# Performance work log

Measured on AMD Instinct MI355X. Metric: run time of the kernel, lower is better.

## Reference

```python
import jax, jax.numpy as jnp
import numpy as np

SPACE_TOKEN = 63
STRIDE = 2
B, F, T, W = 16, 512, 8192, 4096


def setup_inputs() -> dict:
    key = jax.random.key(0)
    k1, k2, k3 = jax.random.split(key, 3)
    word_preds = jax.random.normal(k1, (B, F, W), dtype=jnp.float32)
    char_features = jax.random.normal(k2, (B, F, T), dtype=jnp.float32)
    target_chars = jax.random.randint(k3, (B, T), 0, 64, dtype=jnp.int32)
    return {"word_preds": word_preds, "char_features": char_features, "target_chars": target_chars}


def _per_batch(wp, cf, ch):
    # wp: (F, W) predicted word vectors; cf: (F, T) char features; ch: (T,) char ids
    Tn = ch.shape[0]
    Wn = wp.shape[1]
    space = ch == SPACE_TOKEN
    cum = jnp.cumsum(space.astype(jnp.int32))  # spaces seen up to and including t
    n_spaces = cum[-1]
    # span k lives strictly between space #k and space #(k+1) (0-indexed spaces).
    # a non-space char at t (with cum[t] spaces before it) belongs to span cum[t]-1.
    seg = jnp.where(space | (cum == 0), Tn, cum - 1)  # invalid chars -> dump segment Tn
    counts = jax.ops.segment_sum(jnp.ones((Tn,), jnp.int32), seg, num_segments=Tn + 1)[:Tn]
    sums = jax.ops.segment_sum(cf.T, seg, num_segments=Tn + 1)[:Tn]  # (Tn, F)
    # position of space #k via one-hot scatter of positions
    sid = jnp.where(space, cum - 1, Tn)
    pos_k = jax.ops.segment_sum(jnp.arange(Tn, dtype=jnp.int32), sid, num_segments=Tn + 1)[:Tn]
    word_pos = pos_k // STRIDE
    k = jnp.arange(Tn, dtype=jnp.int32)
    # valid span: a following space exists, span non-empty, word_pos in range
    valid = (k < n_spaces - 1) & (counts > 0) & (word_pos < Wn)
    target = sums / jnp.maximum(counts, 1).astype(sums.dtype)[:, None]  # span mean (detached in torch)
    target = jax.lax.stop_gradient(target)
    pred = wp[:, jnp.clip(word_pos, 0, Wn - 1)].T  # (Tn, F) gather of predictions
    mse = jnp.mean((pred - target) ** 2, axis=1)  # per-span mean over feat dim (F.mse_loss)
    return jnp.sum(jnp.where(valid, mse, 0.0)), jnp.sum(valid.astype(jnp.int32))


def reference(word_preds, char_features, target_chars):
    losses, cnts = jax.vmap(_per_batch)(word_preds, char_features, target_chars)
    total = jnp.sum(losses)
    count = jnp.sum(cnts)
    return jnp.where(count > 0, total / jnp.maximum(count, 1).astype(total.dtype), jnp.float32(0.0))
```

## Files before the change

### kernel.cpp

```cpp
#include <hip/hip_runtime.h>


constexpr int SPACE_TOKEN = 63;
constexpr int B = 16;
constexpr int FDIM = 512;
constexpr int T = 8192;
constexpr int W = 4096;
constexpr int ROWS = 8;
constexpr int NPART = B * FDIM / ROWS;

__global__ __launch_bounds__(1024) void k_find_spaces(
    const int* __restrict__ chars, int* __restrict__ spacePos,
    int* __restrict__ nspaces, int* __restrict__ validCount) {
  const int b = blockIdx.x;
  const int* c = chars + (size_t)b * T;
  int* pos = spacePos + (size_t)b * T;
  __shared__ int s_wtot[16];
  __shared__ int s_wpair[16];
  const int tid = threadIdx.x;
  const int lane = tid & 63;
  const int wid = tid >> 6;

  const int4* c4 = (const int4*)c;
  const int4 a0 = c4[tid * 2];
  const int4 a1 = c4[tid * 2 + 1];
  int v[8] = {a0.x, a0.y, a0.z, a0.w, a1.x, a1.y, a1.z, a1.w};
  int nxt = SPACE_TOKEN + 1;
  if (tid < 1023) nxt = c[tid * 8 + 8];

  int cnt = 0, pairs = 0;
  #pragma unroll
  for (int i = 0; i < 8; ++i) cnt += (v[i] == SPACE_TOKEN);
  #pragma unroll
  for (int i = 0; i < 7; ++i)
    pairs += (v[i] == SPACE_TOKEN) && (v[i + 1] == SPACE_TOKEN);
  pairs += (v[7] == SPACE_TOKEN) && (nxt == SPACE_TOKEN);

  int inc = cnt, pr = pairs;
  #pragma unroll
  for (int o = 1; o < 64; o <<= 1) {
    const int n = __shfl_up(inc, o);
    if (lane >= o) inc += n;
  }
  #pragma unroll
  for (int o = 32; o > 0; o >>= 1) pr += __shfl_down(pr, o);
  if (lane == 63) s_wtot[wid] = inc;
  if (lane == 0) s_wpair[wid] = pr;
  __syncthreads();
  int wexc = 0;
  for (int w = 0; w < wid; ++w) wexc += s_wtot[w];
  int base = wexc + inc - cnt;
  #pragma unroll
  for (int i = 0; i < 8; ++i)
    if (v[i] == SPACE_TOKEN) pos[base++] = tid * 8 + i;
  if (tid == 0) {
    int S = 0, P = 0;
    for (int w = 0; w < 16; ++w) { S += s_wtot[w]; P += s_wpair[w]; }
    nspaces[b] = S;
    validCount[b] = (S > 1 ? S - 1 : 0) - P;
  }
}

__device__ __forceinline__ int swz(int u) { return u ^ ((u >> 3) & 7); }

#define BAR_VM8() do { asm volatile("s_waitcnt vmcnt(8)" ::: "memory"); \
  __builtin_amdgcn_s_barrier(); asm volatile("" ::: "memory"); } while (0)
#define BAR_VM0() do { asm volatile("s_waitcnt vmcnt(0)" ::: "memory"); \
  __builtin_amdgcn_s_barrier(); asm volatile("" ::: "memory"); } while (0)
#define BAR_LGKM() do { asm volatile("s_waitcnt lgkmcnt(0)" ::: "memory"); \
  __builtin_amdgcn_s_barrier(); asm volatile("" ::: "memory"); } while (0)

__device__ __forceinline__ void stage_row(const float4* __restrict__ src,
                                          float* dst, int tid, int wid) {
  float4* d4 = (float4*)dst;
  #pragma unroll
  for (int i = 0; i < 8; ++i) {
    const int u = i * 256 + tid;
    const float4* gsrc = src + swz(u);
    float4* ldst = d4 + (i * 256 + wid * 64);
    __builtin_amdgcn_global_load_lds(
        (const __attribute__((address_space(1))) void*)(const void*)gsrc,
        (__attribute__((address_space(3))) void*)(void*)ldst, 16, 0, 0);
  }
}

__global__ __launch_bounds__(256) void k_span_loss(
    const float* __restrict__ wp, const float* __restrict__ cf,
    const int* __restrict__ spacePos, const int* __restrict__ nspaces,
    float* __restrict__ partials) {
  const int blk = blockIdx.x;
  const int row0 = blk * ROWS;
  const int b = row0 >> 9;
  __shared__ alignas(16) float buf[2][T];
  __shared__ alignas(16) float csum[256];
  __shared__ alignas(16) float cexc[256];
  __shared__ float s_red[4];
  const int tid = threadIdx.x;
  const int lane = tid & 63;
  const int wid = tid >> 6;

  stage_row((const float4*)(cf + (size_t)row0 * T), buf[0], tid, wid);

  const int* pos = spacePos + (size_t)b * T;
  const int S = nspaces[b];
  const int p0r = pos[tid];
  const int p1r = pos[tid + 1];
  const int gidx = (p0r >> 1) & (W - 1);
  float wv[ROWS];
  #pragma unroll
  for (int r = 0; r < ROWS; ++r)
    wv[r] = wp[(size_t)(row0 + r) * W + gidx];

  float acc = 0.f;
  #pragma unroll 1
  for (int r = 0; r < ROWS; ++r) {
    if (r + 1 < ROWS)
      stage_row((const float4*)(cf + (size_t)(row0 + r + 1) * T),
                buf[(r + 1) & 1], tid, wid);
    if (r + 1 < ROWS) { BAR_VM8(); } else { BAR_VM0(); }

    float* rowf = buf[r & 1];
    float4* r4 = (float4*)rowf;

    float4 v[8];
    #pragma unroll
    for (int i = 0; i < 8; ++i) v[i] = r4[swz(tid * 8 + i)];
    float run = 0.f;
    #pragma unroll
    for (int i = 0; i < 8; ++i) {
      v[i].x = (run += v[i].x);
      v[i].y = (run += v[i].y);
      v[i].z = (run += v[i].z);
      v[i].w = (run += v[i].w);
    }
    #pragma unroll
    for (int i = 0; i < 8; ++i) r4[swz(tid * 8 + i)] = v[i];
    csum[tid] = run;
    BAR_LGKM();

    if (tid < 64) {
      const float4 sv = ((const float4*)csum)[tid];
      const float l1 = sv.x + sv.y;
      const float l2 = l1 + sv.z;
      const float tot = l2 + sv.w;
      float inc = tot;
      #pragma unroll
      for (int o = 1; o < 64; o <<= 1) {
        const float n = __shfl_up(inc, o);
        if (tid >= o) inc += n;
      }
      const float exc = inc - tot;
      ((float4*)cexc)[tid] = make_float4(exc, exc + sv.x, exc + l1, exc + l2);
    }
    BAR_LGKM();

    if (tid < S - 1) {
      const int cnt = p1r - p0r - 1;
      if (cnt > 0) {
        const int ta = p1r - 1;
        const float Pa = rowf[(swz(ta >> 2) << 2) | (ta & 3)] + cexc[ta >> 5];
        const float Pb = rowf[(swz(p0r >> 2) << 2) | (p0r & 3)] + cexc[p0r >> 5];
        const float mean = (Pa - Pb) / (float)cnt;
        const float d = wv[r] - mean;
        acc += d * d;
      }
    }
    for (int k = tid + 256; k < S - 1; k += 256) {
      const int p0 = pos[k];
      const int p1 = pos[k + 1];
      const int cnt = p1 - p0 - 1;
      if (cnt > 0) {
        const int ta = p1 - 1;
        const float Pa = rowf[(swz(ta >> 2) << 2) | (ta & 3)] + cexc[ta >> 5];
        const float Pb = rowf[(swz(p0 >> 2) << 2) | (p0 & 3)] + cexc[p0 >> 5];
        const float mean = (Pa - Pb) / (float)cnt;
        const float d = wp[(size_t)(row0 + r) * W + (p0 >> 1)] - mean;
        acc += d * d;
      }
    }
    BAR_LGKM();
  }

  #pragma unroll
  for (int o = 32; o > 0; o >>= 1) acc += __shfl_down(acc, o);
  if (lane == 0) s_red[wid] = acc;
  __syncthreads();
  if (tid == 0) partials[blk] = s_red[0] + s_red[1] + s_red[2] + s_red[3];
}

__global__ __launch_bounds__(256) void k_finalize(
    const float* __restrict__ partials, const int* __restrict__ validCount,
    float* __restrict__ out) {
  __shared__ float s_red[4];
  __shared__ int s_cnt[4];
  const int tid = threadIdx.x;
  const int lane = tid & 63;
  const int wid = tid >> 6;
  float s = 0.f;
  for (int i = tid; i < NPART; i += 256) s += partials[i];
  int cnt = 0;
  for (int i = tid; i < B; i += 256) cnt += validCount[i];
  for (int o = 32; o > 0; o >>= 1) {
    s += __shfl_down(s, o);
    cnt += __shfl_down(cnt, o);
  }
  if (lane == 0) { s_red[wid] = s; s_cnt[wid] = cnt; }
  __syncthreads();
  if (tid == 0) {
    const float total = s_red[0] + s_red[1] + s_red[2] + s_red[3];
    const int c = s_cnt[0] + s_cnt[1] + s_cnt[2] + s_cnt[3];
    out[0] = (c > 0) ? total / ((float)FDIM * (float)c) : 0.f;
  }
}

extern "C" void kernel_launch(void* const* d_in, const int* in_sizes, int n_in,
                              void* d_out, int out_size, void* d_ws, size_t ws_size,
                              hipStream_t stream) {
  const float* wp = (const float*)d_in[0];
  const float* cf = (const float*)d_in[1];
  const int* chars = (const int*)d_in[2];
  float* out = (float*)d_out;

  char* ws = (char*)d_ws;
  int* spacePos = (int*)ws;
  int* nspaces = (int*)(ws + (size_t)B * T * 4);
  int* validCount = nspaces + B;
  float* partials = (float*)(validCount + B);

  k_find_spaces<<<B, 1024, 0, stream>>>(chars, spacePos, nspaces, validCount);
  k_span_loss<<<NPART, 256, 0, stream>>>(wp, cf, spacePos, nspaces, partials);
  k_finalize<<<1, 256, 0, stream>>>(partials, validCount, out);
}
```

Before: 74.37 us.

## Fuse space-finding into span-loss kernel, recomputing space positions per block

Removes the separate space-finding kernel. Each span-loss block now loads its batch's chars, runs a block-wide scan, and keeps only the first 257 space positions in shared memory. This saves a kernel launch and the global spacePos round trip. In exchange, every block repeats the 32 KB char scan, and any span past index 256 falls back to a slow serial rescan of the char row.

```diff
diff --git a/kernel.cpp b/kernel.cpp
--- a/kernel.cpp
+++ b/kernel.cpp
@@ -7,59 +7,8 @@
 constexpr int T = 8192;
 constexpr int W = 4096;
 constexpr int ROWS = 8;
-constexpr int NPART = B * FDIM / ROWS;
-
-__global__ __launch_bounds__(1024) void k_find_spaces(
-    const int* __restrict__ chars, int* __restrict__ spacePos,
-    int* __restrict__ nspaces, int* __restrict__ validCount) {
-  const int b = blockIdx.x;
-  const int* c = chars + (size_t)b * T;
-  int* pos = spacePos + (size_t)b * T;
-  __shared__ int s_wtot[16];
-  __shared__ int s_wpair[16];
-  const int tid = threadIdx.x;
-  const int lane = tid & 63;
-  const int wid = tid >> 6;
-
-  const int4* c4 = (const int4*)c;
-  const int4 a0 = c4[tid * 2];
-  const int4 a1 = c4[tid * 2 + 1];
-  int v[8] = {a0.x, a0.y, a0.z, a0.w, a1.x, a1.y, a1.z, a1.w};
-  int nxt = SPACE_TOKEN + 1;
-  if (tid < 1023) nxt = c[tid * 8 + 8];
-
-  int cnt = 0, pairs = 0;
-  #pragma unroll
-  for (int i = 0; i < 8; ++i) cnt += (v[i] == SPACE_TOKEN);
-  #pragma unroll
-  for (int i = 0; i < 7; ++i)
-    pairs += (v[i] == SPACE_TOKEN) && (v[i + 1] == SPACE_TOKEN);
-  pairs += (v[7] == SPACE_TOKEN) && (nxt == SPACE_TOKEN);
-
-  int inc = cnt, pr = pairs;
-  #pragma unroll
-  for (int o = 1; o < 64; o <<= 1) {
-    const int n = __shfl_up(inc, o);
-    if (lane >= o) inc += n;
-  }
-  #pragma unroll
-  for (int o = 32; o > 0; o >>= 1) pr += __shfl_down(pr, o);
-  if (lane == 63) s_wtot[wid] = inc;
-  if (lane == 0) s_wpair[wid] = pr;
-  __syncthreads();
-  int wexc = 0;
-  for (int w = 0; w < wid; ++w) wexc += s_wtot[w];
-  int base = wexc + inc - cnt;
-  #pragma unroll
-  for (int i = 0; i < 8; ++i)
-    if (v[i] == SPACE_TOKEN) pos[base++] = tid * 8 + i;
-  if (tid == 0) {
-    int S = 0, P = 0;
-    for (int w = 0; w < 16; ++w) { S += s_wtot[w]; P += s_wpair[w]; }
-    nspaces[b] = S;
-    validCount[b] = (S > 1 ? S - 1 : 0) - P;
-  }
-}
+constexpr int NBLK = B * FDIM / ROWS;
+constexpr int SENT = T;
 
 __device__ __forceinline__ int swz(int u) { return u ^ ((u >> 3) & 7); }
 
@@ -84,32 +33,95 @@
   }
 }
 
-__global__ __launch_bounds__(256) void k_span_loss(
+__global__ __launch_bounds__(256) void k_fused(
     const float* __restrict__ wp, const float* __restrict__ cf,
-    const int* __restrict__ spacePos, const int* __restrict__ nspaces,
-    float* __restrict__ partials) {
+    const int* __restrict__ chars, float* __restrict__ partials,
+    int* __restrict__ batchValid) {
   const int blk = blockIdx.x;
   const int row0 = blk * ROWS;
   const int b = row0 >> 9;
   __shared__ alignas(16) float buf[2][T];
   __shared__ alignas(16) float csum[256];
   __shared__ alignas(16) float cexc[256];
+  __shared__ int posL[260];
+  __shared__ int s_wtot[4], s_wpair[4];
   __shared__ float s_red[4];
   const int tid = threadIdx.x;
   const int lane = tid & 63;
   const int wid = tid >> 6;
+  const int* cb = chars + (size_t)b * T;
+
+  int4 creg[8];
+  const int4* c4 = (const int4*)cb;
+  #pragma unroll
+  for (int i = 0; i < 8; ++i) creg[i] = c4[i * 256 + tid];
 
   stage_row((const float4*)(cf + (size_t)row0 * T), buf[0], tid, wid);
 
-  const int* pos = spacePos + (size_t)b * T;
-  const int S = nspaces[b];
-  const int p0r = pos[tid];
-  const int p1r = pos[tid + 1];
+  asm volatile("s_waitcnt vmcnt(8)" ::: "memory");
+
+  int4* b1 = (int4*)buf[1];
+  #pragma unroll
+  for (int i = 0; i < 8; ++i) b1[swz(i * 256 + tid)] = creg[i];
+  posL[tid] = SENT;
+  if (tid == 0) { posL[256] = SENT; posL[257] = SENT; }
+  BAR_LGKM();
+
+  int ch[32];
+  #pragma unroll
+  for (int i = 0; i < 8; ++i) {
+    const int4 q = b1[swz(tid * 8 + i)];
+    ch[i * 4 + 0] = q.x; ch[i * 4 + 1] = q.y;
+    ch[i * 4 + 2] = q.z; ch[i * 4 + 3] = q.w;
+  }
+  int nxt = SPACE_TOKEN + 1;
+  if (tid < 255) nxt = b1[swz((tid + 1) * 8)].x;
+
+  int cnt = 0, pairs = 0;
+  #pragma unroll
+  for (int i = 0; i < 32; ++i) cnt += (ch[i] == SPACE_TOKEN);
+  #pragma unroll
+  for (int i = 0; i < 31; ++i)
+    pairs += (ch[i] == SPACE_TOKEN) && (ch[i + 1] == SPACE_TOKEN);
+  pairs += (ch[31] == SPACE_TOKEN) && (nxt == SPACE_TOKEN);
+
+  int inc = cnt, pr = pairs;
+  #pragma unroll
+  for (int o = 1; o < 64; o <<= 1) {
+    const int n = __shfl_up(inc, o);
+    if (lane >= o) inc += n;
+  }
+  #pragma unroll
+  for (int o = 32; o > 0; o >>= 1) pr += __shfl_down(pr, o);
+  if (lane == 63) s_wtot[wid] = inc;
+  if (lane == 0) s_wpair[wid] = pr;
+  BAR_LGKM();
+
+  int wexc = 0;
+  for (int w = 0; w < wid; ++w) wexc += s_wtot[w];
+  const int S = s_wtot[0] + s_wtot[1] + s_wtot[2] + s_wtot[3];
+  const int P = s_wpair[0] + s_wpair[1] + s_wpair[2] + s_wpair[3];
+  int rk = wexc + inc - cnt;
+  #pragma unroll
+  for (int i = 0; i < 32; ++i)
+    if (ch[i] == SPACE_TOKEN) { if (rk < 257) posL[rk] = tid * 32 + i; ++rk; }
+  BAR_LGKM();
+
+  if ((blk & 63) == 0 && tid == 0)
+    batchValid[b] = (S > 1 ? S - 1 : 0) - P;
+
+  const int p0r = posL[tid];
+  const int p1r = posL[tid + 1];
   const int gidx = (p0r >> 1) & (W - 1);
-  float wv[ROWS];
-  #pragma unroll
-  for (int r = 0; r < ROWS; ++r)
-    wv[r] = wp[(size_t)(row0 + r) * W + gidx];
+  const float* wpb = wp + (size_t)row0 * W + gidx;
+  const float wv0 = wpb[0 * W];
+  const float wv1 = wpb[1 * W];
+  const float wv2 = wpb[2 * W];
+  const float wv3 = wpb[3 * W];
+  const float wv4 = wpb[4 * W];
+  const float wv5 = wpb[5 * W];
+  const float wv6 = wpb[6 * W];
+  const float wv7 = wpb[7 * W];
 
   float acc = 0.f;
   #pragma unroll 1
@@ -143,39 +155,56 @@
       const float l1 = sv.x + sv.y;
       const float l2 = l1 + sv.z;
       const float tot = l2 + sv.w;
-      float inc = tot;
+      float pinc = tot;
       #pragma unroll
       for (int o = 1; o < 64; o <<= 1) {
-        const float n = __shfl_up(inc, o);
-        if (tid >= o) inc += n;
+        const float n = __shfl_up(pinc, o);
+        if (tid >= o) pinc += n;
       }
-      const float exc = inc - tot;
+      const float exc = pinc - tot;
       ((float4*)cexc)[tid] = make_float4(exc, exc + sv.x, exc + l1, exc + l2);
     }
     BAR_LGKM();
 
     if (tid < S - 1) {
-      const int cnt = p1r - p0r - 1;
-      if (cnt > 0) {
+      const int scnt = p1r - p0r - 1;
+      if (scnt > 0) {
         const int ta = p1r - 1;
         const float Pa = rowf[(swz(ta >> 2) << 2) | (ta & 3)] + cexc[ta >> 5];
         const float Pb = rowf[(swz(p0r >> 2) << 2) | (p0r & 3)] + cexc[p0r >> 5];
-        const float mean = (Pa - Pb) / (float)cnt;
-        const float d = wv[r] - mean;
+        const float mean = (Pa - Pb) / (float)scnt;
+        const float wvr = (r == 0) ? wv0 : (r == 1) ? wv1 : (r == 2) ? wv2 :
+                          (r == 3) ? wv3 : (r == 4) ? wv4 : (r == 5) ? wv5 :
+                          (r == 6) ? wv6 : wv7;
+        const float d = wvr - mean;
         acc += d * d;
       }
     }
-    for (int k = tid + 256; k < S - 1; k += 256) {
-      const int p0 = pos[k];
-      const int p1 = pos[k + 1];
-      const int cnt = p1 - p0 - 1;
-      if (cnt > 0) {
-        const int ta = p1 - 1;
-        const float Pa = rowf[(swz(ta >> 2) << 2) | (ta & 3)] + cexc[ta >> 5];
-        const float Pb = rowf[(swz(p0 >> 2) << 2) | (p0 & 3)] + cexc[p0 >> 5];
-        const float mean = (Pa - Pb) / (float)cnt;
-        const float d = wp[(size_t)(row0 + r) * W + (p0 >> 1)] - mean;
-        acc += d * d;
+    if (S - 1 > 256) {
+      int want = 256 + tid;
+      if (want < S - 1) {
+        int rank2 = 0;
+        int p0 = -1;
+        for (int t = 0; t < T; ++t) {
+          if (cb[t] == SPACE_TOKEN) {
+            if (rank2 == want) {
+              p0 = t;
+            } else if (rank2 == want + 1) {
+              const int scnt = t - p0 - 1;
+              if (scnt > 0) {
+                const int ta = t - 1;
+                const float Pa = rowf[(swz(ta >> 2) << 2) | (ta & 3)] + cexc[ta >> 5];
+                const float Pb = rowf[(swz(p0 >> 2) << 2) | (p0 & 3)] + cexc[p0 >> 5];
+                const float mean = (Pa - Pb) / (float)scnt;
+                const float d = wp[(size_t)(row0 + r) * W + (p0 >> 1)] - mean;
+                acc += d * d;
+              }
+              want += 256;
+              if (want >= S - 1) break;
+            }
+            rank2++;
+          }
+        }
       }
     }
     BAR_LGKM();
@@ -189,7 +218,7 @@
 }
 
 __global__ __launch_bounds__(256) void k_finalize(
-    const float* __restrict__ partials, const int* __restrict__ validCount,
+    const float* __restrict__ partials, const int* __restrict__ batchValid,
     float* __restrict__ out) {
   __shared__ float s_red[4];
   __shared__ int s_cnt[4];
@@ -197,9 +226,9 @@
   const int lane = tid & 63;
   const int wid = tid >> 6;
   float s = 0.f;
-  for (int i = tid; i < NPART; i += 256) s += partials[i];
+  for (int i = tid; i < NBLK; i += 256) s += partials[i];
   int cnt = 0;
-  for (int i = tid; i < B; i += 256) cnt += validCount[i];
+  for (int i = tid; i < B; i += 256) cnt += batchValid[i];
   for (int o = 32; o > 0; o >>= 1) {
     s += __shfl_down(s, o);
     cnt += __shfl_down(cnt, o);
@@ -222,12 +251,9 @@
   float* out = (float*)d_out;
 
   char* ws = (char*)d_ws;
-  int* spacePos = (int*)ws;
-  int* nspaces = (int*)(ws + (size_t)B * T * 4);
-  int* validCount = nspaces + B;
-  float* partials = (float*)(validCount + B);
-
-  k_find_spaces<<<B, 1024, 0, stream>>>(chars, spacePos, nspaces, validCount);
-  k_span_loss<<<NPART, 256, 0, stream>>>(wp, cf, spacePos, nspaces, partials);
-  k_finalize<<<1, 256, 0, stream>>>(partials, validCount, out);
-}
+  float* partials = (float*)ws;
+  int* batchValid = (int*)(ws + NBLK * 4);
+
+  k_fused<<<NBLK, 256, 0, stream>>>(wp, cf, chars, partials, batchValid);
+  k_finalize<<<1, 256, 0, stream>>>(partials, batchValid, out);
+}
```

New measurement: 72.47 us. 1.03x faster.
